# Kernel optimization log

Measured on AMD Instinct MI355X. Metric: run time of the kernel, lower is better.

The kernel has to match this reference:

```python
import jax, jax.numpy as jnp
import numpy as np

EPS = 1e-6
NHEAD = 12

def _ln(x):
    m = jnp.mean(x, -1, keepdims=True)
    v = jnp.var(x, -1, keepdims=True)
    return (x - m) * jax.lax.rsqrt(v + EPS)

def _modulate(x, shift, scale):
    return x * (1 + scale[:, None, :]) + shift[:, None, :]

def _pos_embedding(idx, dim, max_len=2048):
    K = jnp.arange(dim // 2)
    ang = idx[..., None] * jnp.pi / (max_len ** (2.0 * K / dim))
    return jnp.concatenate([jnp.sin(ang), jnp.cos(ang)], axis=-1)

def _forward(x, W_xemb, b_xemb, ds_table, sg_table, Wqkv, bqkv, Wo, bo, W1, b1, W2, b2,
             Wada, bada, Wada_f, bada_f, W_out, dataset, spacegroup, mask):
    B, N, _ = x.shape
    D = W_xemb.shape[1]
    hd = D // NHEAD
    # conditioning vector: label embeddings (eval mode: no cfg dropout)
    c = ds_table[dataset] + sg_table[spacegroup]                 # [B, D]
    h = x @ W_xemb + b_xemb + _pos_embedding(jnp.arange(N), D)[None]  # [B, N, D]
    kmask = mask[:, None, None, :]                                # [B,1,1,N], True = padded key
    scale_qk = 1.0 / jnp.sqrt(jnp.asarray(hd, h.dtype))

    def block(h, p):
        Wqkv, bqkv, Wo, bo, W1, b1, W2, b2, Wada, bada = p
        mods = jax.nn.silu(c) @ Wada + bada                      # [B, 6D]
        sh_a, sc_a, g_a, sh_m, sc_m, g_m = jnp.split(mods, 6, axis=-1)
        xm = _modulate(_ln(h), sh_a, sc_a)
        qkv = (xm @ Wqkv + bqkv).reshape(B, N, 3, NHEAD, hd)
        q, k, v = qkv[:, :, 0], qkv[:, :, 1], qkv[:, :, 2]
        scores = jnp.einsum('bqhd,bkhd->bhqk', q, k) * scale_qk   # MATH-backend path: full [B,H,N,N]
        scores = jnp.where(kmask, -jnp.inf, scores)
        attn = jax.nn.softmax(scores, axis=-1)
        o = jnp.einsum('bhqk,bkhd->bqhd', attn, v).reshape(B, N, D)
        o = o @ Wo + bo
        h = h + g_a[:, None, :] * o
        y = _modulate(_ln(h), sh_m, sc_m)
        y = jax.nn.gelu(y @ W1 + b1, approximate=True) @ W2 + b2
        h = h + g_m[:, None, :] * y
        return h, None

    h, _ = jax.lax.scan(block, h, (Wqkv, bqkv, Wo, bo, W1, b1, W2, b2, Wada, bada))
    mods_f = jax.nn.silu(c) @ Wada_f + bada_f
    sh_f, sc_f = jnp.split(mods_f, 2, axis=-1)
    return _modulate(_ln(h), sh_f, sc_f) @ W_out                  # [B, N, 1] per-token energy


def setup_inputs() -> dict:
    B, N, D, L, DX, HID = 32, 512, 768, 12, 8, 3072
    keys = iter(jax.random.split(jax.random.key(0), 32))
    def w(shape, s=0.02):
        return jax.random.normal(next(keys), shape, jnp.float32) * s
    return dict(
        x=jax.random.normal(next(keys), (B, N, 2 * DX), jnp.float32),
        W_xemb=w((2 * DX, D)), b_xemb=jnp.zeros((D,), jnp.float32),
        ds_table=w((3, D)), sg_table=w((231, D)),
        Wqkv=w((L, D, 3 * D)), bqkv=jnp.zeros((L, 3 * D), jnp.float32),
        Wo=w((L, D, D)), bo=jnp.zeros((L, D), jnp.float32),
        W1=w((L, D, HID)), b1=jnp.zeros((L, HID), jnp.float32),
        W2=w((L, HID, D)), b2=jnp.zeros((L, D), jnp.float32),
        Wada=w((L, D, 6 * D)), bada=jnp.zeros((L, 6 * D), jnp.float32),
        Wada_f=w((D, 2 * D)), bada_f=jnp.zeros((2 * D,), jnp.float32),
        W_out=w((D, 1)),
        dataset=jax.random.randint(next(keys), (32,), 0, 2),
        spacegroup=jax.random.randint(next(keys), (32,), 0, 230),
        mask=jax.random.bernoulli(next(keys), 0.1, (32, 512)),
    )


def reference(x, W_xemb, b_xemb, ds_table, sg_table, Wqkv, bqkv, Wo, bo, W1, b1, W2, b2,
              Wada, bada, Wada_f, bada_f, W_out, dataset, spacegroup, mask):
    return _forward(x, W_xemb, b_xemb, ds_table, sg_table, Wqkv, bqkv, Wo, bo, W1, b1,
                    W2, b2, Wada, bada, Wada_f, bada_f, W_out, dataset, spacegroup, mask)
```

## Files before the change

kernel.cpp:

```cpp
#include <hip/hip_runtime.h>
#include <hip/hip_bf16.h>

#define B_   32
#define N_   512
#define D_   768
#define H_   12
#define HID_ 3072
#define L_   12
#define M_   (B_*N_)

typedef __attribute__((ext_vector_type(8))) short short8_t;
typedef __attribute__((ext_vector_type(4))) short short4_t;
typedef __attribute__((ext_vector_type(4))) float f32x4;
typedef __hip_bfloat16 bf16;

__device__ __forceinline__ void gll16(const void* g, void* l){
    __builtin_amdgcn_global_load_lds((const __attribute__((address_space(1))) void*)g,
                                     (__attribute__((address_space(3))) void*)l, 16, 0, 0);
}

__global__ __launch_bounds__(256) void embed_kernel(
    const float* __restrict__ x, const float* __restrict__ Wx,
    const float* __restrict__ bx, float* __restrict__ h)
{
    long idx = (long)blockIdx.x * 256 + threadIdx.x;
    int d = (int)(idx % 768);
    long m = idx / 768;
    int n = (int)(m % 512);
    float acc = bx[d];
    const float* xr = x + m * 16;
    #pragma unroll
    for (int k = 0; k < 16; ++k) acc = fmaf(xr[k], Wx[k*768 + d], acc);
    int K = (d < 384) ? d : d - 384;
    float ang = (float)n * 3.14159265358979323846f * expf(-(2.0f*(float)K/768.0f) * 7.624618986159398f);
    acc += (d < 384) ? sinf(ang) : cosf(ang);
    h[idx] = acc;
}

__global__ __launch_bounds__(256) void csilu_kernel(
    const float* __restrict__ ds_t, const float* __restrict__ sg_t,
    const int* __restrict__ dataset, const int* __restrict__ sg, float* __restrict__ out)
{
    int idx = blockIdx.x*256 + threadIdx.x;
    int b = idx / 768, d = idx % 768;
    float c = ds_t[dataset[b]*768 + d] + sg_t[sg[b]*768 + d];
    out[idx] = c / (1.0f + expf(-c));
}

__global__ __launch_bounds__(256) void mods_part_kernel(
    const float* __restrict__ csilu, const float* __restrict__ W,
    float* __restrict__ part, int Nd2, long wLayerStride)
{
    __shared__ float cs[16][96];
    int n2 = blockIdx.x*256 + threadIdx.x;
    int l = blockIdx.y, z = blockIdx.z;
    int kz = z >> 1, bg = z & 1;
    int L = gridDim.y;
    for (int t = threadIdx.x; t < 16*96; t += 256){
        int bb = t / 96, kk = t - bb*96;
        cs[bb][kk] = csilu[(bg*16 + bb)*768 + kz*96 + kk];
    }
    __syncthreads();
    const float2* Wl = (const float2*)(W + (long)l*wLayerStride);
    float2 acc[16];
    #pragma unroll
    for (int b=0;b<16;b++) acc[b] = make_float2(0.f, 0.f);
    for (int k=0;k<96;++k){
        float2 wv = Wl[(long)(kz*96 + k)*Nd2 + n2];
        #pragma unroll
        for (int b=0;b<16;b++){
            float c = cs[b][k];
            acc[b].x = fmaf(c, wv.x, acc[b].x);
            acc[b].y = fmaf(c, wv.y, acc[b].y);
        }
    }
    float2* pp = (float2*)part + ((long)(kz*L + l)*32 + bg*16)*Nd2 + n2;
    #pragma unroll
    for (int b=0;b<16;b++) pp[(long)b*Nd2] = acc[b];
}

__global__ __launch_bounds__(256) void mods_reduce_kernel(
    const float* __restrict__ part, const float* __restrict__ bias,
    float* __restrict__ out, int Nd, int L)
{
    long idx = (long)blockIdx.x*256 + threadIdx.x;
    int n = (int)(idx % Nd);
    long r = idx / Nd;
    int b = (int)(r & 31);
    int l = (int)(r >> 5);
    float s = bias[(long)l*Nd + n];
    #pragma unroll
    for (int z=0;z<8;z++) s += part[((long)(z*L + l)*32 + b)*Nd + n];
    out[idx] = s;
}

__global__ __launch_bounds__(256) void transpose4_kernel(
    const float* __restrict__ Wqkv, const float* __restrict__ Wo,
    const float* __restrict__ W1,  const float* __restrict__ W2,
    bf16* __restrict__ wqT, bf16* __restrict__ woT,
    bf16* __restrict__ w1T, bf16* __restrict__ w2T)
{
    __shared__ float t[32][33];
    int tt = blockIdx.x;
    const float* src; bf16* dst; int K, Nd, nx;
    if (tt < 1728){ src=Wqkv; dst=wqT; K=768; Nd=2304; nx=72; }
    else if (tt < 2304){ src=Wo; dst=woT; K=768; Nd=768; nx=24; tt -= 1728; }
    else if (tt < 4608){ src=W1; dst=w1T; K=768; Nd=3072; nx=96; tt -= 2304; }
    else { src=W2; dst=w2T; K=3072; Nd=768; nx=24; tt -= 4608; }
    int n0 = (tt % nx)*32, k0 = (tt / nx)*32;
    int tx = threadIdx.x & 31, ty = threadIdx.x >> 5;
    #pragma unroll
    for (int j=0;j<4;j++)
        t[ty + j*8][tx] = src[(long)(k0 + ty + j*8)*Nd + n0 + tx];
    __syncthreads();
    #pragma unroll
    for (int j=0;j<4;j++)
        dst[(long)(n0 + ty + j*8)*K + k0 + tx] = __float2bfloat16(t[tx][ty + j*8]);
}

__global__ __launch_bounds__(256) void ln_mod_kernel(
    const float* __restrict__ h, const float* __restrict__ shiftB,
    const float* __restrict__ scaleB, int modsStride, bf16* __restrict__ out)
{
    int wave = threadIdx.x >> 6, lane = threadIdx.x & 63;
    long row = (long)blockIdx.x*4 + wave;
    int b = (int)(row >> 9);
    const float4* xr = (const float4*)(h + row*768);
    float4 v[3];
    float s = 0.f, ss = 0.f;
    #pragma unroll
    for (int i=0;i<3;i++){
        v[i] = xr[lane + i*64];
        s  += v[i].x + v[i].y + v[i].z + v[i].w;
        ss += v[i].x*v[i].x + v[i].y*v[i].y + v[i].z*v[i].z + v[i].w*v[i].w;
    }
    #pragma unroll
    for (int o=1;o<64;o<<=1){ s += __shfl_xor(s,o,64); ss += __shfl_xor(ss,o,64); }
    float mean = s * (1.0f/768.0f);
    float var  = ss * (1.0f/768.0f) - mean*mean;
    float rstd = rsqrtf(var + 1e-6f);
    const float4* sh4 = (const float4*)(shiftB + (long)b*modsStride);
    const float4* sc4 = (const float4*)(scaleB + (long)b*modsStride);
    short4_t* orow = (short4_t*)(out + row*768);
    #pragma unroll
    for (int i=0;i<3;i++){
        float4 sh = sh4[lane + i*64];
        float4 sc = sc4[lane + i*64];
        float o0 = (v[i].x-mean)*rstd*(1.f+sc.x) + sh.x;
        float o1 = (v[i].y-mean)*rstd*(1.f+sc.y) + sh.y;
        float o2 = (v[i].z-mean)*rstd*(1.f+sc.z) + sh.z;
        float o3 = (v[i].w-mean)*rstd*(1.f+sc.w) + sh.w;
        bf16 b0 = __float2bfloat16(o0), b1 = __float2bfloat16(o1);
        bf16 b2 = __float2bfloat16(o2), b3 = __float2bfloat16(o3);
        short4_t pk;
        pk[0] = *(short*)&b0; pk[1] = *(short*)&b1;
        pk[2] = *(short*)&b2; pk[3] = *(short*)&b3;
        orow[lane + i*64] = pk;
    }
}

__device__ __forceinline__ float gelu_f(float x){
    float z2 = 1.5957691216057308f * x * (1.0f + 0.044715f*x*x);
    return x / (1.0f + __expf(-z2));
}

template<int MODE>
__global__ __launch_bounds__(512, 2) void gemm256_kernel(
    const bf16* __restrict__ A, const bf16* __restrict__ Bw,
    const float* __restrict__ bias, bf16* __restrict__ outBf,
    float* __restrict__ hres, const float* __restrict__ gate,
    int Nd, int Kd, int gateStride)
{
    __shared__ __align__(16) short lds[65536];
    int tid = threadIdx.x;
    int lane = tid & 63, wave = tid >> 6;
    int frow = lane & 15, g = lane >> 4;
    int wm = wave >> 2, wn4 = wave & 3;

    int nwg = gridDim.x;
    int bid = blockIdx.x;
    int q8  = nwg >> 3;
    int wgid = (bid & 7) * q8 + (bid >> 3);
    int ntiles = Nd >> 8;
    int mt = wgid / ntiles, ct = wgid - mt*ntiles;
    int m0 = mt * 256, n0 = ct * 256;

    const short* Ag = (const short*)A;
    const short* Bg = (const short*)Bw;
    int r0 = tid >> 3;
    int s0 = (tid & 7) ^ (r0 & 7);
    const short* aSrc = Ag + (long)(m0 + r0)*Kd + s0*8;
    const short* bSrc = Bg + (long)(n0 + r0)*Kd + s0*8;
    long r64 = (long)64*Kd;
    int wb = wave*512;

    int aRd = wm*4096 + frow*64;
    int bRd = wn4*2048 + frow*64;
    int slotK0 = (g ^ (frow & 7))*8;
    int slotK1 = ((4+g) ^ (frow & 7))*8;

    f32x4 acc[8][4];
    #pragma unroll
    for (int i=0;i<8;i++)
        #pragma unroll
        for (int j=0;j<4;j++) acc[i][j] = (f32x4){0.f,0.f,0.f,0.f};

    short8_t af[4][2];
    short8_t bf[2][2];

    int NT = Kd >> 6;

#define STA(kt, h) { \
    short* d_ = &lds[((kt)&1)*16384 + (h)*8192 + wb]; \
    const short* s_ = aSrc + (long)(h)*2*r64 + (long)(kt)*64; \
    gll16(s_, d_); gll16(s_ + r64, d_ + 4096); }
#define STB(kt, h) { \
    short* d_ = &lds[32768 + ((kt)&1)*16384 + (h)*8192 + wb]; \
    const short* s_ = bSrc + (long)(h)*2*r64 + (long)(kt)*64; \
    gll16(s_, d_); gll16(s_ + r64, d_ + 4096); }

#define RDA(mh) { \
    int ba_ = pA + (mh)*8192 + aRd; \
    _Pragma("unroll") \
    for (int i=0;i<4;++i){ \
        af[i][0] = *(const short8_t*)&lds[ba_ + i*1024 + slotK0]; \
        af[i][1] = *(const short8_t*)&lds[ba_ + i*1024 + slotK1]; } }
#define RDB(nh) { \
    int bb_ = pB + (nh)*8192 + bRd; \
    _Pragma("unroll") \
    for (int j=0;j<2;++j){ \
        bf[j][0] = *(const short8_t*)&lds[bb_ + j*1024 + slotK0]; \
        bf[j][1] = *(const short8_t*)&lds[bb_ + j*1024 + slotK1]; } }

#define MFMA16(mh, nh) { \
    __builtin_amdgcn_s_setprio(1); \
    _Pragma("unroll") \
    for (int kh=0;kh<2;++kh) \
        _Pragma("unroll") \
        for (int i=0;i<4;++i) \
            _Pragma("unroll") \
            for (int j=0;j<2;++j) \
                acc[(mh)*4+i][(nh)*2+j] = __builtin_amdgcn_mfma_f32_16x16x32_bf16( \
                    af[i][kh], bf[j][kh], acc[(mh)*4+i][(nh)*2+j], 0, 0, 0); \
    __builtin_amdgcn_s_setprio(0); }

    STA(0,0); STB(0,0); STB(0,1); STA(0,1);
    asm volatile("s_waitcnt vmcnt(4)" ::: "memory");
    __builtin_amdgcn_s_barrier();
    __builtin_amdgcn_sched_barrier(0);

    for (int kt=0; kt<NT; ++kt){
        int pA = (kt&1)*16384;
        int pB = 32768 + (kt&1)*16384;
        bool pf = (kt+1 < NT);

        RDA(0); RDB(0);
        if (pf) STA(kt+1, 0);
        __builtin_amdgcn_s_barrier();
        __builtin_amdgcn_sched_barrier(0);
        MFMA16(0, 0);
        __builtin_amdgcn_sched_barrier(0);
        if (pf) asm volatile("s_waitcnt vmcnt(4)" ::: "memory");
        else    asm volatile("s_waitcnt vmcnt(2)" ::: "memory");
        __builtin_amdgcn_s_barrier();
        __builtin_amdgcn_sched_barrier(0);

        RDB(1);
        if (pf) STB(kt+1, 0);
        __builtin_amdgcn_s_barrier();
        __builtin_amdgcn_sched_barrier(0);
        MFMA16(0, 1);
        __builtin_amdgcn_sched_barrier(0);
        if (pf) asm volatile("s_waitcnt vmcnt(4)" ::: "memory");
        else    asm volatile("s_waitcnt vmcnt(0)" ::: "memory");
        __builtin_amdgcn_s_barrier();
        __builtin_amdgcn_sched_barrier(0);

        RDA(1);
        if (pf) STB(kt+1, 1);
        __builtin_amdgcn_s_barrier();
        __builtin_amdgcn_sched_barrier(0);
        MFMA16(1, 1);
        __builtin_amdgcn_sched_barrier(0);
        __builtin_amdgcn_s_barrier();
        __builtin_amdgcn_sched_barrier(0);

        RDB(0);
        if (pf) STA(kt+1, 1);
        __builtin_amdgcn_s_barrier();
        __builtin_amdgcn_sched_barrier(0);
        MFMA16(1, 0);
        __builtin_amdgcn_sched_barrier(0);
        if (pf) asm volatile("s_waitcnt vmcnt(4)" ::: "memory");
        __builtin_amdgcn_s_barrier();
        __builtin_amdgcn_sched_barrier(0);
    }
#undef STA
#undef STB
#undef RDA
#undef RDB
#undef MFMA16

    int rb = m0 + wm*64 + g*4;
    int cb = n0 + wn4*32 + frow;
    float bv0 = bias[cb], bv1 = bias[cb+16], bv2 = bias[cb+128], bv3 = bias[cb+144];
    #pragma unroll
    for (int mh=0; mh<2; ++mh){
        #pragma unroll
        for (int i=0;i<4;++i){
            #pragma unroll
            for (int r=0;r<4;++r){
                int row = rb + mh*128 + i*16 + r;
                float v0 = acc[mh*4+i][0][r] + bv0;
                float v1 = acc[mh*4+i][1][r] + bv1;
                float v2 = acc[mh*4+i][2][r] + bv2;
                float v3 = acc[mh*4+i][3][r] + bv3;
                if (MODE == 0){
                    bf16* o_ = outBf + (long)row*Nd + cb;
                    o_[0]   = __float2bfloat16(v0);
                    o_[16]  = __float2bfloat16(v1);
                    o_[128] = __float2bfloat16(v2);
                    o_[144] = __float2bfloat16(v3);
                } else if (MODE == 1){
                    bf16* o_ = outBf + (long)row*Nd + cb;
                    o_[0]   = __float2bfloat16(gelu_f(v0));
                    o_[16]  = __float2bfloat16(gelu_f(v1));
                    o_[128] = __float2bfloat16(gelu_f(v2));
                    o_[144] = __float2bfloat16(gelu_f(v3));
                } else {
                    int bb = row >> 9;
                    const float* gp = gate + (long)bb*gateStride + cb;
                    float* hp = hres + (long)row*768 + cb;
                    hp[0]   += gp[0]   * v0;
                    hp[16]  += gp[16]  * v1;
                    hp[128] += gp[128] * v2;
                    hp[144] += gp[144] * v3;
                }
            }
        }
    }
}

__global__ __launch_bounds__(256) void attn_mfma_kernel(
    const bf16* __restrict__ qkv, const int* __restrict__ mask, bf16* __restrict__ o)
{
    __shared__ __align__(16) short Ks[64][72];
    __shared__ __align__(16) short Vt[64][72];
    __shared__ __align__(16) short Ps[4][16][72];
    __shared__ float maskf[512];
    int tid = threadIdx.x, lane = tid & 63, wave = tid >> 6;
    int qt = blockIdx.x, hh = blockIdx.y, b = blockIdx.z;
    long base = (long)b * 512 * 2304;
    const short* qkvs = (const short*)qkv;

    maskf[tid]       = mask[b*512 + tid]       ? -1e30f : 0.0f;
    maskf[tid + 256] = mask[b*512 + tid + 256] ? -1e30f : 0.0f;

    int c = lane & 15, g = lane >> 4;
    int qrowA = qt*64 + wave*16 + c;
    const short* qptr = qkvs + base + (long)qrowA*2304 + hh*64 + g*8;
    short8_t qa0 = *(const short8_t*)qptr;
    short8_t qa1 = *(const short8_t*)(qptr + 32);

    f32x4 oacc[4];
    #pragma unroll
    for (int j=0;j<4;j++) oacc[j] = (f32x4){0.f,0.f,0.f,0.f};
    float m_r[4], l_r[4];
    #pragma unroll
    for (int r=0;r<4;r++){ m_r[r] = -50.0f; l_r[r] = 0.0f; }

    int kp = (tid & 31)*2, gv = tid >> 5;
    const short* kgbase = qkvs + base + 768  + hh*64;
    const short* vgbase = qkvs + base + 1536 + hh*64 + gv*8;

    for (int kt=0; kt<8; ++kt){
        __syncthreads();
        {
            int v0 = tid, v1 = tid + 256;
            int r0 = v0>>3, c0 = (v0&7)*8, r1 = v1>>3, c1 = (v1&7)*8;
            *(short8_t*)&Ks[r0][c0] = *(const short8_t*)(kgbase + (long)(kt*64 + r0)*2304 + c0);
            *(short8_t*)&Ks[r1][c1] = *(const short8_t*)(kgbase + (long)(kt*64 + r1)*2304 + c1);
            short8_t va = *(const short8_t*)(vgbase + (long)(kt*64 + kp    )*2304);
            short8_t vb = *(const short8_t*)(vgbase + (long)(kt*64 + kp + 1)*2304);
            #pragma unroll
            for (int e=0;e<8;e++){
                unsigned int pack = (unsigned int)(unsigned short)va[e]
                                  | ((unsigned int)(unsigned short)vb[e] << 16);
                *(unsigned int*)&Vt[gv*8 + e][kp] = pack;
            }
        }
        __syncthreads();
        f32x4 s[4];
        #pragma unroll
        for (int j=0;j<4;j++){
            short8_t kb0 = *(const short8_t*)&Ks[j*16 + c][g*8];
            short8_t kb1 = *(const short8_t*)&Ks[j*16 + c][g*8 + 32];
            f32x4 z = (f32x4){0.f,0.f,0.f,0.f};
            z = __builtin_amdgcn_mfma_f32_16x16x32_bf16(qa0, kb0, z, 0, 0, 0);
            z = __builtin_amdgcn_mfma_f32_16x16x32_bf16(qa1, kb1, z, 0, 0, 0);
            s[j] = z;
        }
        #pragma unroll
        for (int j=0;j<4;j++){
            float mbj = maskf[kt*64 + j*16 + c];
            #pragma unroll
            for (int r=0;r<4;r++) s[j][r] = s[j][r]*0.125f + mbj;
        }
        #pragma unroll
        for (int r=0;r<4;r++){
            float tm = fmaxf(fmaxf(s[0][r], s[1][r]), fmaxf(s[2][r], s[3][r]));
            #pragma unroll
            for (int o_=1;o_<16;o_<<=1) tm = fmaxf(tm, __shfl_xor(tm, o_, 64));
            float mn  = fmaxf(m_r[r], tm);
            float fac = __expf(m_r[r] - mn);
            m_r[r] = mn;
            float ls = l_r[r]*fac;
            #pragma unroll
            for (int j=0;j<4;j++){
                float p = __expf(s[j][r] - mn);
                s[j][r] = p;
                ls += p;
            }
            l_r[r] = ls;
            #pragma unroll
            for (int j=0;j<4;j++) oacc[j][r] *= fac;
        }
        #pragma unroll
        for (int j=0;j<4;j++)
            #pragma unroll
            for (int r=0;r<4;r++)
                *(bf16*)&Ps[wave][g*4 + r][j*16 + c] = __float2bfloat16(s[j][r]);
        short8_t pa0 = *(const short8_t*)&Ps[wave][c][g*8];
        short8_t pa1 = *(const short8_t*)&Ps[wave][c][g*8 + 32];
        #pragma unroll
        for (int j=0;j<4;j++){
            short8_t vb0 = *(const short8_t*)&Vt[j*16 + c][g*8];
            short8_t vb1 = *(const short8_t*)&Vt[j*16 + c][g*8 + 32];
            oacc[j] = __builtin_amdgcn_mfma_f32_16x16x32_bf16(pa0, vb0, oacc[j], 0, 0, 0);
            oacc[j] = __builtin_amdgcn_mfma_f32_16x16x32_bf16(pa1, vb1, oacc[j], 0, 0, 0);
        }
    }
    #pragma unroll
    for (int r=0;r<4;r++){
        float lt = l_r[r];
        #pragma unroll
        for (int o_=1;o_<16;o_<<=1) lt += __shfl_xor(lt, o_, 64);
        l_r[r] = 1.0f / lt;
    }
    int qrowC = qt*64 + wave*16 + g*4;
    bf16* orow = o + ((long)b*512 + qrowC)*768 + hh*64;
    #pragma unroll
    for (int r=0;r<4;r++)
        #pragma unroll
        for (int j=0;j<4;j++)
            orow[(long)r*768 + j*16 + c] = __float2bfloat16(oacc[j][r] * l_r[r]);
}

__global__ __launch_bounds__(256) void outdot_kernel(
    const bf16* __restrict__ xm, const float* __restrict__ Wout, float* __restrict__ out)
{
    int tid=threadIdx.x, lane=tid&63, wave=tid>>6;
    long row = (long)blockIdx.x*4 + wave;
    const bf16* xr = xm + row*768;
    float acc = 0.f;
    #pragma unroll
    for (int i=0;i<12;i++){ int d = lane + i*64; acc = fmaf(__bfloat162float(xr[d]), Wout[d], acc); }
    #pragma unroll
    for (int o_=1;o_<64;o_<<=1) acc += __shfl_xor(acc, o_, 64);
    if (lane==0) out[row] = acc;
}

extern "C" void kernel_launch(void* const* d_in, const int* in_sizes, int n_in,
                              void* d_out, int out_size, void* d_ws, size_t ws_size,
                              hipStream_t stream)
{
    const float* x      = (const float*)d_in[0];
    const float* W_xemb = (const float*)d_in[1];
    const float* b_xemb = (const float*)d_in[2];
    const float* ds_t   = (const float*)d_in[3];
    const float* sg_t   = (const float*)d_in[4];
    const float* Wqkv   = (const float*)d_in[5];
    const float* bqkv   = (const float*)d_in[6];
    const float* Wo     = (const float*)d_in[7];
    const float* bo     = (const float*)d_in[8];
    const float* W1     = (const float*)d_in[9];
    const float* b1     = (const float*)d_in[10];
    const float* W2     = (const float*)d_in[11];
    const float* b2     = (const float*)d_in[12];
    const float* Wada   = (const float*)d_in[13];
    const float* bada   = (const float*)d_in[14];
    const float* Wada_f = (const float*)d_in[15];
    const float* bada_f = (const float*)d_in[16];
    const float* W_out  = (const float*)d_in[17];
    const int* dataset  = (const int*)d_in[18];
    const int* sgroup   = (const int*)d_in[19];
    const int* mask     = (const int*)d_in[20];
    float* out = (float*)d_out;

    char* ws = (char*)d_ws;
    size_t off = 0;
    auto alloc = [&](size_t bytes)->void*{
        void* p = ws + off; off += (bytes + 255) & ~(size_t)255; return p; };
    float* h     = (float*)alloc((size_t)M_*768*4);
    float* csilu = (float*)alloc((size_t)32*768*4);
    float* modsA = (float*)alloc((size_t)12*32*4608*4);
    float* modsF = (float*)alloc((size_t)32*1536*4);
    bf16*  xm    = (bf16*) alloc((size_t)M_*768*2);
    bf16*  wbuf  = (bf16*) alloc((size_t)7077888*2);
    bf16*  big   = (bf16*) alloc((size_t)M_*3072*2);
    bf16* qkvb = big;
    bf16* y1   = big;
    float* partA = (float*)big;
    float* partF = partA + (size_t)8*12*32*4608;
    bf16* wqT = wbuf;
    bf16* woT = wqT + 2304*768;
    bf16* w1T = woT + 768*768;
    bf16* w2T = w1T + 3072*768;

    embed_kernel<<<49152, 256, 0, stream>>>(x, W_xemb, b_xemb, h);
    csilu_kernel<<<96, 256, 0, stream>>>(ds_t, sg_t, dataset, sgroup, csilu);
    mods_part_kernel<<<dim3(9,12,16), 256, 0, stream>>>(csilu, Wada, partA, 2304, (long)768*4608);
    mods_reduce_kernel<<<6912, 256, 0, stream>>>(partA, bada, modsA, 4608, 12);
    mods_part_kernel<<<dim3(3,1,16), 256, 0, stream>>>(csilu, Wada_f, partF, 768, 0);
    mods_reduce_kernel<<<192, 256, 0, stream>>>(partF, bada_f, modsF, 1536, 1);

    for (int l=0; l<12; ++l){
        const float* modsL = modsA + (long)l*32*4608;
        transpose4_kernel<<<6912, 256, 0, stream>>>(
            Wqkv + (long)l*768*2304, Wo + (long)l*768*768,
            W1 + (long)l*768*3072,  W2 + (long)l*3072*768,
            wqT, woT, w1T, w2T);

        ln_mod_kernel<<<4096, 256, 0, stream>>>(h, modsL + 0*768, modsL + 1*768, 4608, xm);
        gemm256_kernel<0><<<576, 512, 0, stream>>>(xm, wqT, bqkv + l*2304, qkvb,
                                                   nullptr, nullptr, 2304, 768, 0);
        attn_mfma_kernel<<<dim3(8, 12, 32), 256, 0, stream>>>(qkvb, mask, xm);
        gemm256_kernel<2><<<192, 512, 0, stream>>>(xm, woT, bo + l*768, nullptr,
                                                   h, modsL + 2*768, 768, 768, 4608);
        ln_mod_kernel<<<4096, 256, 0, stream>>>(h, modsL + 3*768, modsL + 4*768, 4608, xm);
        gemm256_kernel<1><<<768, 512, 0, stream>>>(xm, w1T, b1 + l*3072, y1,
                                                   nullptr, nullptr, 3072, 768, 0);
        gemm256_kernel<2><<<192, 512, 0, stream>>>(y1, w2T, b2 + l*768, nullptr,
                                                   h, modsL + 5*768, 768, 3072, 4608);
    }
    ln_mod_kernel<<<4096, 256, 0, stream>>>(h, modsF + 0, modsF + 768, 1536, xm);
    outdot_kernel<<<4096, 256, 0, stream>>>(xm, W_out, out);
}
```

Measured before the change: 5.346 ms.

## Add 128x192-tile GEMM for QKV, out-proj and FC2; trim barriers in 256 GEMM

Adds a new 256-thread GEMM kernel with 128x192 output tiles, XCD-aware block mapping and a double-buffered direct-to-LDS load pipeline. It replaces the 256x256 GEMM for the QKV, attention output and FC2 projections. The N=768 GEMMs previously launched only 192 workgroups, so the smaller tiles give more workgroups and better CU occupancy. The change also removes one barrier per phase in the existing 256-tile GEMM's main loop, which still serves FC1. That cuts sync overhead but may open LDS read/write race windows.

Result: faster. 4.818 ms (-9.9%).

```diff
diff --git a/kernel.cpp b/kernel.cpp
--- a/kernel.cpp
+++ b/kernel.cpp
@@ -165,6 +165,143 @@
 }
 
 template<int MODE>
+__global__ __launch_bounds__(256, 2) void gemm128_kernel(
+    const bf16* __restrict__ A, const bf16* __restrict__ Bw,
+    const float* __restrict__ bias, bf16* __restrict__ outBf,
+    float* __restrict__ hres, const float* __restrict__ gate,
+    int Nd, int Kd, int gateStride)
+{
+    __shared__ __align__(16) short lds[40960];
+    int tid = threadIdx.x;
+    int lane = tid & 63, wave = tid >> 6;
+    int frow = lane & 15, g = lane >> 4;
+
+    int nx = gridDim.x;
+    int bid = blockIdx.y * nx + blockIdx.x;
+    int xcd = bid & 7;
+    int wq  = bid >> 3;
+    int mt  = xcd * 16 + (wq & 15);
+    int ct  = wq >> 4;
+    int m0 = mt * 128, n0 = ct * 192;
+    int wn = wave * 48;
+
+    const short* Ag = (const short*)A;
+    const short* Bg = (const short*)Bw;
+    int r0 = tid >> 3, s0 = (tid & 7) ^ ((tid >> 3) & 7);
+    const short* aSrc = Ag + (long)(m0 + r0)*Kd + s0*8;
+    const short* bSrc = Bg + (long)(n0 + r0)*Kd + s0*8;
+    long rj = (long)32*Kd;
+    int wbase = wave*512;
+
+    int aFrag = frow*64;
+    int bFrag = (wn + frow)*64;
+    int slotK0 = (g ^ (frow & 7))*8;
+    int slotK1 = ((4+g) ^ (frow & 7))*8;
+
+    f32x4 acc[8][3];
+    #pragma unroll
+    for (int i=0;i<8;i++)
+        #pragma unroll
+        for (int j=0;j<3;j++) acc[i][j] = (f32x4){0.f,0.f,0.f,0.f};
+
+    int NT = Kd >> 6;
+
+#define STAGE(kt, ps) { \
+    int par_ = (kt)&1; \
+    if ((ps)==0){ \
+        short* d_ = &lds[par_*8192 + wbase]; \
+        gll16(aSrc +        (long)(kt)*64, d_); \
+        gll16(aSrc +   rj + (long)(kt)*64, d_ + 2048); \
+        gll16(aSrc + 2*rj + (long)(kt)*64, d_ + 4096); \
+        gll16(aSrc + 3*rj + (long)(kt)*64, d_ + 6144); \
+    } else { \
+        short* d_ = &lds[16384 + par_*12288 + wbase]; \
+        gll16(bSrc +        (long)(kt)*64, d_); \
+        gll16(bSrc +   rj + (long)(kt)*64, d_ + 2048); \
+        gll16(bSrc + 2*rj + (long)(kt)*64, d_ + 4096); \
+        gll16(bSrc + 3*rj + (long)(kt)*64, d_ + 6144); \
+        gll16(bSrc + 4*rj + (long)(kt)*64, d_ + 8192); \
+        gll16(bSrc + 5*rj + (long)(kt)*64, d_ + 10240); \
+    } }
+
+    STAGE(0,0); STAGE(0,1);
+
+    for (int kt=0; kt<NT; ++kt){
+        int pA  = (kt&1)*8192;
+        int pBb = 16384 + (kt&1)*12288;
+        bool pf = (kt+1 < NT);
+        if (pf){
+            STAGE(kt+1, 0);
+            asm volatile("s_waitcnt vmcnt(4)" ::: "memory");
+        } else {
+            asm volatile("s_waitcnt vmcnt(0)" ::: "memory");
+        }
+        __builtin_amdgcn_s_barrier();
+        __builtin_amdgcn_sched_barrier(0);
+        short8_t af[8], bfr[3];
+        #pragma unroll
+        for (int i=0;i<8;i++) af[i]  = *(const short8_t*)&lds[pA + aFrag + i*1024 + slotK0];
+        #pragma unroll
+        for (int j=0;j<3;j++) bfr[j] = *(const short8_t*)&lds[pBb + bFrag + j*1024 + slotK0];
+        if (pf) STAGE(kt+1, 1);
+        __builtin_amdgcn_s_setprio(1);
+        #pragma unroll
+        for (int i=0;i<8;i++)
+            #pragma unroll
+            for (int j=0;j<3;j++)
+                acc[i][j] = __builtin_amdgcn_mfma_f32_16x16x32_bf16(af[i], bfr[j], acc[i][j], 0, 0, 0);
+        __builtin_amdgcn_s_setprio(0);
+        #pragma unroll
+        for (int i=0;i<8;i++) af[i]  = *(const short8_t*)&lds[pA + aFrag + i*1024 + slotK1];
+        #pragma unroll
+        for (int j=0;j<3;j++) bfr[j] = *(const short8_t*)&lds[pBb + bFrag + j*1024 + slotK1];
+        __builtin_amdgcn_s_setprio(1);
+        #pragma unroll
+        for (int i=0;i<8;i++)
+            #pragma unroll
+            for (int j=0;j<3;j++)
+                acc[i][j] = __builtin_amdgcn_mfma_f32_16x16x32_bf16(af[i], bfr[j], acc[i][j], 0, 0, 0);
+        __builtin_amdgcn_s_setprio(0);
+        __builtin_amdgcn_sched_barrier(0);
+        __builtin_amdgcn_s_barrier();
+        __builtin_amdgcn_sched_barrier(0);
+    }
+#undef STAGE
+
+    int rbase = m0 + g*4;
+    int cbase = n0 + wn + frow;
+    float bv0 = bias[cbase], bv1 = bias[cbase+16], bv2 = bias[cbase+32];
+    #pragma unroll
+    for (int i=0;i<8;i++){
+        #pragma unroll
+        for (int r=0;r<4;r++){
+            int row = rbase + i*16 + r;
+            float v0 = acc[i][0][r] + bv0;
+            float v1 = acc[i][1][r] + bv1;
+            float v2 = acc[i][2][r] + bv2;
+            if (MODE == 0){
+                bf16* o_ = outBf + (long)row*Nd + cbase;
+                o_[0]  = __float2bfloat16(v0);
+                o_[16] = __float2bfloat16(v1);
+                o_[32] = __float2bfloat16(v2);
+            } else if (MODE == 1){
+                bf16* o_ = outBf + (long)row*Nd + cbase;
+                o_[0]  = __float2bfloat16(gelu_f(v0));
+                o_[16] = __float2bfloat16(gelu_f(v1));
+                o_[32] = __float2bfloat16(gelu_f(v2));
+            } else {
+                int bb = row >> 9;
+                const float* gp = gate + (long)bb*gateStride + cbase;
+                float* hp = hres + (long)row*768 + cbase;
+                hp[0]  += gp[0]  * v0;
+                hp[16] += gp[16] * v1;
+                hp[32] += gp[32] * v2;
+            }
+        }
+    }
+}
+
+template<int MODE>
 __global__ __launch_bounds__(512, 2) void gemm256_kernel(
     const bf16* __restrict__ A, const bf16* __restrict__ Bw,
     const float* __restrict__ bias, bf16* __restrict__ outBf,
@@ -256,10 +393,8 @@
 
         RDA(0); RDB(0);
         if (pf) STA(kt+1, 0);
-        __builtin_amdgcn_s_barrier();
         __builtin_amdgcn_sched_barrier(0);
         MFMA16(0, 0);
-        __builtin_amdgcn_sched_barrier(0);
         if (pf) asm volatile("s_waitcnt vmcnt(4)" ::: "memory");
         else    asm volatile("s_waitcnt vmcnt(2)" ::: "memory");
         __builtin_amdgcn_s_barrier();
@@ -267,10 +402,8 @@
 
         RDB(1);
         if (pf) STB(kt+1, 0);
-        __builtin_amdgcn_s_barrier();
         __builtin_amdgcn_sched_barrier(0);
         MFMA16(0, 1);
-        __builtin_amdgcn_sched_barrier(0);
         if (pf) asm volatile("s_waitcnt vmcnt(4)" ::: "memory");
         else    asm volatile("s_waitcnt vmcnt(0)" ::: "memory");
         __builtin_amdgcn_s_barrier();
@@ -278,19 +411,15 @@
 
         RDA(1);
         if (pf) STB(kt+1, 1);
-        __builtin_amdgcn_s_barrier();
         __builtin_amdgcn_sched_barrier(0);
         MFMA16(1, 1);
-        __builtin_amdgcn_sched_barrier(0);
         __builtin_amdgcn_s_barrier();
         __builtin_amdgcn_sched_barrier(0);
 
         RDB(0);
         if (pf) STA(kt+1, 1);
-        __builtin_amdgcn_s_barrier();
         __builtin_amdgcn_sched_barrier(0);
         MFMA16(1, 0);
-        __builtin_amdgcn_sched_barrier(0);
         if (pf) asm volatile("s_waitcnt vmcnt(4)" ::: "memory");
         __builtin_amdgcn_s_barrier();
         __builtin_amdgcn_sched_barrier(0);
@@ -532,16 +661,16 @@
             wqT, woT, w1T, w2T);
 
         ln_mod_kernel<<<4096, 256, 0, stream>>>(h, modsL + 0*768, modsL + 1*768, 4608, xm);
-        gemm256_kernel<0><<<576, 512, 0, stream>>>(xm, wqT, bqkv + l*2304, qkvb,
-                                                   nullptr, nullptr, 2304, 768, 0);
+        gemm128_kernel<0><<<dim3(12, 128), 256, 0, stream>>>(xm, wqT, bqkv + l*2304, qkvb,
+                                                             nullptr, nullptr, 2304, 768, 0);
         attn_mfma_kernel<<<dim3(8, 12, 32), 256, 0, stream>>>(qkvb, mask, xm);
-        gemm256_kernel<2><<<192, 512, 0, stream>>>(xm, woT, bo + l*768, nullptr,
-                                                   h, modsL + 2*768, 768, 768, 4608);
+        gemm128_kernel<2><<<dim3(4, 128), 256, 0, stream>>>(xm, woT, bo + l*768, nullptr,
+                                                            h, modsL + 2*768, 768, 768, 4608);
         ln_mod_kernel<<<4096, 256, 0, stream>>>(h, modsL + 3*768, modsL + 4*768, 4608, xm);
         gemm256_kernel<1><<<768, 512, 0, stream>>>(xm, w1T, b1 + l*3072, y1,
                                                    nullptr, nullptr, 3072, 768, 0);
-        gemm256_kernel<2><<<192, 512, 0, stream>>>(y1, w2T, b2 + l*768, nullptr,
-                                                   h, modsL + 5*768, 768, 3072, 4608);
+        gemm128_kernel<2><<<dim3(4, 128), 256, 0, stream>>>(y1, w2T, b2 + l*768, nullptr,
+                                                            h, modsL + 5*768, 768, 3072, 4608);
     }
     ln_mod_kernel<<<4096, 256, 0, stream>>>(h, modsF + 0, modsF + 768, 1536, xm);
     outdot_kernel<<<4096, 256, 0, stream>>>(xm, W_out, out);
```
